# Performance work log

Measured on AMD Instinct MI355X. Metric: run time of the kernel, lower is better.

The kernel has to match this reference:

```python
import jax, jax.numpy as jnp
import numpy as np

N = 100000
E = 1600000
IN_DIM = 128
OUT_DIM = 64


def setup_inputs() -> dict:
    key = jax.random.key(0)
    k_h, k_ei, k_ew, k_W, k_a = jax.random.split(key, 5)
    h = jax.random.normal(k_h, (N, IN_DIM), dtype=jnp.float32)
    edge_index = jax.random.randint(k_ei, (2, E), 0, N, dtype=jnp.int64)
    edge_weight = jax.random.uniform(k_ew, (E,), dtype=jnp.float32)
    # nn.Linear weights (Kaiming-uniform-ish scale)
    W = jax.random.uniform(k_W, (OUT_DIM, IN_DIM), dtype=jnp.float32,
                           minval=-1.0, maxval=1.0) / np.sqrt(IN_DIM)
    a = jax.random.uniform(k_a, (2 * OUT_DIM,), dtype=jnp.float32,
                           minval=-1.0, maxval=1.0) / np.sqrt(2 * OUT_DIM)
    return {"h": h, "edge_index": edge_index, "edge_weight": edge_weight,
            "W": W, "a": a}


def reference(h, edge_index, edge_weight, W, a):
    # Faithful translation of _GATConvSparse.forward (inference; dropout = identity).
    n = h.shape[0]
    src, dst = edge_index[0], edge_index[1]
    Wh = h @ W.T                                  # (N, out_dim)
    d = Wh.shape[1]
    # a(cat([Wh[src], Wh[dst]])) == Wh[src] @ a[:d] + Wh[dst] @ a[d:]
    alpha = Wh[src] @ a[:d] + Wh[dst] @ a[d:]     # (E,)
    alpha = alpha * edge_weight
    # Buggy-but-faithful 'softmax': segment-sum raw scores onto dst nodes...
    alpha_node = jax.ops.segment_sum(alpha, dst, num_segments=n)   # (N,)
    alpha_exp = jnp.exp(alpha_node - alpha_node.max())             # (N,)
    # ...then normalize per-edge exp(src) by sum of exp(src) over each dst segment.
    denom = jax.ops.segment_sum(alpha_exp[src], dst, num_segments=n)  # (N,)
    alpha_norm = alpha_exp[src] / (denom[dst] + 1e-9)              # (E,)
    out = jax.ops.segment_sum(alpha_norm[:, None] * Wh[src], dst,
                              num_segments=n)                      # (N, out_dim)
    return jax.nn.elu(out)
```

## Files before the change

kernel.cpp:

```cpp
#include <hip/hip_runtime.h>
#include <math.h>

#define Nn 100000
#define Ee 1600000
#define IND 128
#define OUTD 64
#define DPB 64
#define NB 1563
#define BSTR 1536
#define CAP 1536
#define GB 1563
#define EB_BLOCKS 391
#define AFIX 1048576.0f

using bf16x8 = __attribute__((ext_vector_type(8))) short;
using f32x4 = __attribute__((ext_vector_type(4))) float;

__device__ __forceinline__ unsigned short f2bf(float f) {
    unsigned u = __float_as_uint(f);
    u = u + 0x7FFFu + ((u >> 16) & 1u);
    return (unsigned short)(u >> 16);
}
__device__ __forceinline__ float bf2f(unsigned short h) {
    return __uint_as_float(((unsigned)h) << 16);
}

__device__ __forceinline__ bool probe64(const void* __restrict__ ei) {
    const long long* p = (const long long*)ei;
    bool ok = true;
#pragma unroll
    for (int i = 0; i < 8; ++i) {
        long long v = p[i];
        ok = ok && (v >= 0 && v < Nn);
    }
    return ok;
}

__device__ __forceinline__ void load_edge(const void* ei, int e, bool is64,
                                          int& s, int& d) {
    if (is64) {
        const long long* p = (const long long*)ei;
        s = (int)p[e];
        d = (int)p[Ee + e];
    } else {
        const int* p = (const int*)ei;
        s = p[e];
        d = p[Ee + e];
    }
}

__global__ __launch_bounds__(256) void k_fused(
    const float* __restrict__ h, const float* __restrict__ W,
    const float* __restrict__ a, unsigned short* __restrict__ Whb,
    float* __restrict__ s1, float* __restrict__ s2) {
    __shared__ unsigned short Ash[64][136];
    __shared__ unsigned short Wsh[64][136];
    __shared__ float al[2 * OUTD];
    int bid = blockIdx.x;
    int t = threadIdx.x;

    int R = bid * 64;
    for (int i = t; i < 2048; i += 256) {
        float4 v = ((const float4*)W)[i];
        int r = i >> 5, c = (i & 31) << 2;
        unsigned lo = (unsigned)f2bf(v.x) | ((unsigned)f2bf(v.y) << 16);
        unsigned hi = (unsigned)f2bf(v.z) | ((unsigned)f2bf(v.w) << 16);
        *(uint2*)&Wsh[r][c] = make_uint2(lo, hi);
    }
    if (t < 32) ((float4*)al)[t] = ((const float4*)a)[t];
    for (int i = t; i < 2048; i += 256) {
        int r = i >> 5, c = (i & 31) << 2;
        int n = R + r;
        float4 v = make_float4(0.f, 0.f, 0.f, 0.f);
        if (n < Nn) v = ((const float4*)(h + (size_t)n * IND))[i & 31];
        unsigned lo = (unsigned)f2bf(v.x) | ((unsigned)f2bf(v.y) << 16);
        unsigned hi = (unsigned)f2bf(v.z) | ((unsigned)f2bf(v.w) << 16);
        *(uint2*)&Ash[r][c] = make_uint2(lo, hi);
    }
    __syncthreads();

    int w = t >> 6, l = t & 63;
    int li = l & 15, lg = l >> 4;
    f32x4 acc[4];
#pragma unroll
    for (int nt = 0; nt < 4; ++nt) acc[nt] = (f32x4){0.f, 0.f, 0.f, 0.f};
#pragma unroll
    for (int kk = 0; kk < 4; ++kk) {
        bf16x8 af = *(const bf16x8*)&Ash[w * 16 + li][kk * 32 + lg * 8];
#pragma unroll
        for (int nt = 0; nt < 4; ++nt) {
            bf16x8 bf = *(const bf16x8*)&Wsh[nt * 16 + li][kk * 32 + lg * 8];
            acc[nt] = __builtin_amdgcn_mfma_f32_16x16x32_bf16(af, bf,
                                                              acc[nt],
                                                              0, 0, 0);
        }
    }
    float p1[4] = {0.f, 0.f, 0.f, 0.f};
    float p2[4] = {0.f, 0.f, 0.f, 0.f};
#pragma unroll
    for (int nt = 0; nt < 4; ++nt) {
        float a1v = al[nt * 16 + li];
        float a2v = al[OUTD + nt * 16 + li];
#pragma unroll
        for (int r = 0; r < 4; ++r) {
            float v = acc[nt][r];
            p1[r] += v * a1v;
            p2[r] += v * a2v;
            int row = R + w * 16 + lg * 4 + r;
            if (row < Nn)
                Whb[(size_t)row * OUTD + nt * 16 + li] = f2bf(v);
        }
    }
#pragma unroll
    for (int r = 0; r < 4; ++r) {
#pragma unroll
        for (int m = 1; m < 16; m <<= 1) {
            p1[r] += __shfl_xor(p1[r], m, 64);
            p2[r] += __shfl_xor(p2[r], m, 64);
        }
    }
    if (li < 4) {
        int row = R + w * 16 + lg * 4 + li;
        if (row < Nn) {
            s1[row] = p1[li];
            s2[row] = p2[li];
        }
    }
}

__global__ __launch_bounds__(512) void k_binscatter(
    const void* __restrict__ ei, const float* __restrict__ ew,
    const float* __restrict__ s1, const float* __restrict__ s2,
    int* __restrict__ bcursor, uint2* __restrict__ bins) {
    __shared__ int cnt[NB];
    __shared__ int gbase[NB];
    for (int i = threadIdx.x; i < NB; i += 512) cnt[i] = 0;
    __syncthreads();
    bool is64 = probe64(ei);
    int base = blockIdx.x * 4096;
    unsigned rx[8];
    int ryi[8];
    int rb[8];
    int rk[8];
#pragma unroll
    for (int i = 0; i < 8; ++i) {
        int e = base + i * 512 + threadIdx.x;
        rb[i] = -1;
        rx[i] = 0;
        ryi[i] = 0;
        rk[i] = 0;
        if (e < Ee) {
            int s, d;
            load_edge(ei, e, is64, s, d);
            float alpha = (s1[s] + s2[d]) * ew[e];
            ryi[i] = (int)rintf(alpha * AFIX);
            int b = d >> 6;
            rb[i] = b;
            rk[i] = atomicAdd(&cnt[b], 1);
            rx[i] = ((unsigned)s << 7) | ((unsigned)(d & 63) << 24);
        }
    }
    __syncthreads();
    for (int i = threadIdx.x; i < NB; i += 512) {
        int c = cnt[i];
        if (c) gbase[i] = atomicAdd(bcursor + i, c);
    }
    __syncthreads();
#pragma unroll
    for (int i = 0; i < 8; ++i) {
        if (rb[i] >= 0) {
            int pos = gbase[rb[i]] + rk[i];
            if (pos < BSTR)
                bins[(size_t)rb[i] * BSTR + pos] =
                    make_uint2(rx[i], (unsigned)ryi[i]);
        }
    }
}

__global__ __launch_bounds__(256) void k_balpha(
    const uint2* __restrict__ bins, const int* __restrict__ bcnt,
    float* __restrict__ ae) {
    __shared__ int anl[DPB];
    int b = blockIdx.x;
    int t = threadIdx.x;
    if (t < DPB) anl[t] = 0;
    __syncthreads();
    int e0 = b * BSTR;
    int c = bcnt[b];
    int e1 = e0 + (c < BSTR ? c : BSTR);
    for (int k = e0 + t; k < e1; k += 256) {
        uint2 r = bins[k];
        atomicAdd(&anl[r.x >> 24], (int)r.y);
    }
    __syncthreads();
    if (t < DPB) {
        int n = b * DPB + t;
        if (n < Nn) ae[n] = expf((float)anl[t] * (1.f / AFIX));
    }
}

#define AGG_BODY(NR)                                                         \
    {                                                                        \
        uint2 rr[NR];                                                        \
        unsigned ww[NR];                                                     \
        _Pragma("unroll") for (int j = 0; j < NR; ++j)                       \
            rr[j] = lp[2 * j];                                               \
        _Pragma("unroll") for (int j = 0; j < NR; ++j)                       \
            ww[j] = *(const unsigned*)(whbB + (rr[j].x + hl4));              \
        _Pragma("unroll") for (int j = 0; j < NR; ++j) {                     \
            float aa = __uint_as_float(rr[j].y);                             \
            acc.x += aa * __uint_as_float(ww[j] << 16);                      \
            acc.y += aa * __uint_as_float(ww[j] & 0xFFFF0000u);              \
            den += aa;                                                       \
        }                                                                    \
        lp += 2 * NR;                                                        \
    }

__global__ __launch_bounds__(512, 4) void k_agg(
    const uint2* __restrict__ bins, const int* __restrict__ bcnt,
    const float* __restrict__ ae, const unsigned short* __restrict__ Whb,
    float* __restrict__ out) {
    __shared__ uint2 lrec[CAP];
    __shared__ int cnt[DPB];
    __shared__ int sbase[DPB];
    int b = blockIdx.x;
    int t = threadIdx.x;
    int lane = t & 63;
    int wave = t >> 6;
    int half = lane >> 5;
    int hl = lane & 31;
    unsigned hl4 = (unsigned)hl << 2;
    int e0 = b * BSTR;
    int c = bcnt[b];
    int total = c < BSTR ? c : BSTR;
    int e1 = e0 + total;
    const char* whbB = (const char*)Whb;

    if (t < DPB) cnt[t] = 0;
    __syncthreads();

    unsigned su[CAP / 512];
    float sa[CAP / 512];
    int srk[CAP / 512];
#pragma unroll
    for (int i = 0; i < CAP / 512; ++i) {
        int k = e0 + i * 512 + t;
        srk[i] = -1;
        if (k < e1) {
            uint2 r = bins[k];
            srk[i] = atomicAdd(&cnt[r.x >> 24], 1);
            su[i] = r.x;
            sa[i] = ae[(r.x >> 7) & 0x1FFFF];
        }
    }
    __syncthreads();
    if (t < DPB) {
        int v = cnt[t];
#pragma unroll
        for (int d = 1; d < DPB; d <<= 1) {
            int u = __shfl_up(v, d, 64);
            if (t >= d) v += u;
        }
        sbase[t] = v;
    }
    __syncthreads();
#pragma unroll
    for (int i = 0; i < CAP / 512; ++i) {
        if (srk[i] >= 0) {
            int dloc = su[i] >> 24;
            int pos = sbase[dloc] - cnt[dloc] + srk[i];
            lrec[pos] = make_uint2(su[i] & 0x00FFFF80u,
                                   __float_as_uint(sa[i]));
        }
    }
    __syncthreads();

    for (int d = wave * 8; d < wave * 8 + 8; ++d) {
        int k1 = sbase[d];
        int k = k1 - cnt[d];
        const uint2* lp = lrec + k + half;
        float2 acc = make_float2(0.f, 0.f);
        float den = 0.f;
        for (; k + 15 < k1; k += 16) AGG_BODY(8);
        for (; k + 7 < k1; k += 8) AGG_BODY(4);
        for (; k + 1 < k1; k += 2) AGG_BODY(1);
        if (k < k1) {
            uint2 rA = lrec[k];
            unsigned wA = *(const unsigned*)(whbB + (rA.x + hl4));
            float aA = half ? 0.f : __uint_as_float(rA.y);
            acc.x += aA * __uint_as_float(wA << 16);
            acc.y += aA * __uint_as_float(wA & 0xFFFF0000u);
            den += aA;
        }
        float ax = acc.x + __shfl_xor(acc.x, 32, 64);
        float ay = acc.y + __shfl_xor(acc.y, 32, 64);
        float dn = den + __shfl_xor(den, 32, 64);
        if (half == 0) {
            int n = b * DPB + d;
            if (n < Nn) {
                float inv = 1.f / (dn + 1e-9f);
                float vx = ax * inv;
                float vy = ay * inv;
                vx = vx > 0.f ? vx : expm1f(vx);
                vy = vy > 0.f ? vy : expm1f(vy);
                *(float2*)&out[(size_t)n * OUTD + hl * 2] =
                    make_float2(vx, vy);
            }
        }
    }
}

extern "C" void kernel_launch(void* const* d_in, const int* in_sizes, int n_in,
                              void* d_out, int out_size, void* d_ws,
                              size_t ws_size, hipStream_t stream) {
    const float* h = (const float*)d_in[0];
    const void* ei = d_in[1];
    const float* ew = (const float*)d_in[2];
    const float* W = (const float*)d_in[3];
    const float* a = (const float*)d_in[4];
    float* out = (float*)d_out;

    unsigned short* Whb = (unsigned short*)d_ws;
    float* s1 = (float*)(Whb + (size_t)Nn * OUTD);
    float* s2 = s1 + Nn;
    float* ae = s2 + Nn;
    int* bcursor = (int*)(ae + Nn);
    uint2* bins = (uint2*)(bcursor + 2048);

    hipMemsetAsync(bcursor, 0, 2048 * sizeof(int), stream);

    k_fused<<<GB, 256, 0, stream>>>(h, W, a, Whb, s1, s2);
    k_binscatter<<<EB_BLOCKS, 512, 0, stream>>>(ei, ew, s1, s2, bcursor, bins);
    k_balpha<<<NB, 256, 0, stream>>>(bins, bcursor, ae);
    k_agg<<<NB, 512, 0, stream>>>(bins, bcursor, ae, Whb, out);
}
```

Baseline: 107.6 us.

## Replace atomic bin cursors with a deterministic count-then-scan binning pass

Adds a histogram pass, fused into the matmul kernel as extra blocks, that counts edges per destination bin for each chunk. A new column-wise scan kernel turns those counts into per-chunk offsets, so the scatter kernel reads precomputed bases instead of doing global atomicAdds on shared cursors. This also removes the memset and shrinks the per-bin stride, giving a smaller bins buffer. The cost is an extra kernel launch, a second read of the destination indices, and a counts buffer in workspace.

```diff
diff --git a/kernel.cpp b/kernel.cpp
--- a/kernel.cpp
+++ b/kernel.cpp
@@ -7,10 +7,11 @@
 #define OUTD 64
 #define DPB 64
 #define NB 1563
-#define BSTR 1536
+#define BSTR 1280
 #define CAP 1536
 #define GB 1563
 #define EB_BLOCKS 391
+#define CSCAN_BLOCKS 196
 #define AFIX 1048576.0f
 
 using bf16x8 = __attribute__((ext_vector_type(8))) short;
@@ -49,95 +50,144 @@
     }
 }
 
+__device__ __forceinline__ int load_dst(const void* ei, int e, bool is64) {
+    if (is64) return (int)((const long long*)ei)[Ee + e];
+    return ((const int*)ei)[Ee + e];
+}
+
 __global__ __launch_bounds__(256) void k_fused(
     const float* __restrict__ h, const float* __restrict__ W,
     const float* __restrict__ a, unsigned short* __restrict__ Whb,
-    float* __restrict__ s1, float* __restrict__ s2) {
+    float* __restrict__ s1, float* __restrict__ s2,
+    const void* __restrict__ ei, unsigned short* __restrict__ counts) {
     __shared__ unsigned short Ash[64][136];
     __shared__ unsigned short Wsh[64][136];
     __shared__ float al[2 * OUTD];
     int bid = blockIdx.x;
     int t = threadIdx.x;
 
-    int R = bid * 64;
-    for (int i = t; i < 2048; i += 256) {
-        float4 v = ((const float4*)W)[i];
-        int r = i >> 5, c = (i & 31) << 2;
-        unsigned lo = (unsigned)f2bf(v.x) | ((unsigned)f2bf(v.y) << 16);
-        unsigned hi = (unsigned)f2bf(v.z) | ((unsigned)f2bf(v.w) << 16);
-        *(uint2*)&Wsh[r][c] = make_uint2(lo, hi);
-    }
-    if (t < 32) ((float4*)al)[t] = ((const float4*)a)[t];
-    for (int i = t; i < 2048; i += 256) {
-        int r = i >> 5, c = (i & 31) << 2;
-        int n = R + r;
-        float4 v = make_float4(0.f, 0.f, 0.f, 0.f);
-        if (n < Nn) v = ((const float4*)(h + (size_t)n * IND))[i & 31];
-        unsigned lo = (unsigned)f2bf(v.x) | ((unsigned)f2bf(v.y) << 16);
-        unsigned hi = (unsigned)f2bf(v.z) | ((unsigned)f2bf(v.w) << 16);
-        *(uint2*)&Ash[r][c] = make_uint2(lo, hi);
-    }
-    __syncthreads();
-
-    int w = t >> 6, l = t & 63;
-    int li = l & 15, lg = l >> 4;
-    f32x4 acc[4];
-#pragma unroll
-    for (int nt = 0; nt < 4; ++nt) acc[nt] = (f32x4){0.f, 0.f, 0.f, 0.f};
-#pragma unroll
-    for (int kk = 0; kk < 4; ++kk) {
-        bf16x8 af = *(const bf16x8*)&Ash[w * 16 + li][kk * 32 + lg * 8];
+    if (bid < GB) {
+        int R = bid * 64;
+        for (int i = t; i < 2048; i += 256) {
+            float4 v = ((const float4*)W)[i];
+            int r = i >> 5, c = (i & 31) << 2;
+            unsigned lo = (unsigned)f2bf(v.x) | ((unsigned)f2bf(v.y) << 16);
+            unsigned hi = (unsigned)f2bf(v.z) | ((unsigned)f2bf(v.w) << 16);
+            *(uint2*)&Wsh[r][c] = make_uint2(lo, hi);
+        }
+        if (t < 32) ((float4*)al)[t] = ((const float4*)a)[t];
+        for (int i = t; i < 2048; i += 256) {
+            int r = i >> 5, c = (i & 31) << 2;
+            int n = R + r;
+            float4 v = make_float4(0.f, 0.f, 0.f, 0.f);
+            if (n < Nn) v = ((const float4*)(h + (size_t)n * IND))[i & 31];
+            unsigned lo = (unsigned)f2bf(v.x) | ((unsigned)f2bf(v.y) << 16);
+            unsigned hi = (unsigned)f2bf(v.z) | ((unsigned)f2bf(v.w) << 16);
+            *(uint2*)&Ash[r][c] = make_uint2(lo, hi);
+        }
+        __syncthreads();
+
+        int w = t >> 6, l = t & 63;
+        int li = l & 15, lg = l >> 4;
+        f32x4 acc[4];
+#pragma unroll
+        for (int nt = 0; nt < 4; ++nt) acc[nt] = (f32x4){0.f, 0.f, 0.f, 0.f};
+#pragma unroll
+        for (int kk = 0; kk < 4; ++kk) {
+            bf16x8 af = *(const bf16x8*)&Ash[w * 16 + li][kk * 32 + lg * 8];
+#pragma unroll
+            for (int nt = 0; nt < 4; ++nt) {
+                bf16x8 bf = *(const bf16x8*)&Wsh[nt * 16 + li][kk * 32 + lg * 8];
+                acc[nt] = __builtin_amdgcn_mfma_f32_16x16x32_bf16(af, bf,
+                                                                  acc[nt],
+                                                                  0, 0, 0);
+            }
+        }
+        float p1[4] = {0.f, 0.f, 0.f, 0.f};
+        float p2[4] = {0.f, 0.f, 0.f, 0.f};
 #pragma unroll
         for (int nt = 0; nt < 4; ++nt) {
-            bf16x8 bf = *(const bf16x8*)&Wsh[nt * 16 + li][kk * 32 + lg * 8];
-            acc[nt] = __builtin_amdgcn_mfma_f32_16x16x32_bf16(af, bf,
-                                                              acc[nt],
-                                                              0, 0, 0);
-        }
-    }
-    float p1[4] = {0.f, 0.f, 0.f, 0.f};
-    float p2[4] = {0.f, 0.f, 0.f, 0.f};
-#pragma unroll
-    for (int nt = 0; nt < 4; ++nt) {
-        float a1v = al[nt * 16 + li];
-        float a2v = al[OUTD + nt * 16 + li];
+            float a1v = al[nt * 16 + li];
+            float a2v = al[OUTD + nt * 16 + li];
+#pragma unroll
+            for (int r = 0; r < 4; ++r) {
+                float v = acc[nt][r];
+                p1[r] += v * a1v;
+                p2[r] += v * a2v;
+                int row = R + w * 16 + lg * 4 + r;
+                if (row < Nn)
+                    Whb[(size_t)row * OUTD + nt * 16 + li] = f2bf(v);
+            }
+        }
 #pragma unroll
         for (int r = 0; r < 4; ++r) {
-            float v = acc[nt][r];
-            p1[r] += v * a1v;
-            p2[r] += v * a2v;
-            int row = R + w * 16 + lg * 4 + r;
-            if (row < Nn)
-                Whb[(size_t)row * OUTD + nt * 16 + li] = f2bf(v);
-        }
-    }
-#pragma unroll
-    for (int r = 0; r < 4; ++r) {
-#pragma unroll
-        for (int m = 1; m < 16; m <<= 1) {
-            p1[r] += __shfl_xor(p1[r], m, 64);
-            p2[r] += __shfl_xor(p2[r], m, 64);
-        }
-    }
-    if (li < 4) {
-        int row = R + w * 16 + lg * 4 + li;
-        if (row < Nn) {
-            s1[row] = p1[li];
-            s2[row] = p2[li];
-        }
-    }
+#pragma unroll
+            for (int m = 1; m < 16; m <<= 1) {
+                p1[r] += __shfl_xor(p1[r], m, 64);
+                p2[r] += __shfl_xor(p2[r], m, 64);
+            }
+        }
+        if (li < 4) {
+            int row = R + w * 16 + lg * 4 + li;
+            if (row < Nn) {
+                s1[row] = p1[li];
+                s2[row] = p2[li];
+            }
+        }
+    } else {
+        int* cnt = (int*)&Ash[0][0];
+        for (int i = t; i < NB; i += 256) cnt[i] = 0;
+        __syncthreads();
+        bool is64 = probe64(ei);
+        int hc = bid - GB;
+        int base = hc * 4096;
+#pragma unroll
+        for (int i = 0; i < 16; ++i) {
+            int e = base + i * 256 + t;
+            if (e < Ee) atomicAdd(&cnt[load_dst(ei, e, is64) >> 6], 1);
+        }
+        __syncthreads();
+        for (int i = t; i < NB; i += 256)
+            counts[(size_t)hc * NB + i] = (unsigned short)cnt[i];
+    }
+}
+
+__global__ __launch_bounds__(512) void k_cscan(
+    unsigned short* __restrict__ counts, int* __restrict__ bcnt) {
+    int gw = (int)((blockIdx.x * 512 + threadIdx.x) >> 6);
+    int lane = threadIdx.x & 63;
+    if (gw >= NB) return;
+    int run = 0;
+    for (int c0 = 0; c0 < EB_BLOCKS; c0 += 64) {
+        int c = c0 + lane;
+        int v = (c < EB_BLOCKS) ? (int)counts[(size_t)c * NB + gw] : 0;
+        int s = v;
+#pragma unroll
+        for (int d = 1; d < 64; d <<= 1) {
+            int u = __shfl_up(s, d, 64);
+            if (lane >= d) s += u;
+        }
+        if (c < EB_BLOCKS)
+            counts[(size_t)c * NB + gw] = (unsigned short)(run + s - v);
+        run += __shfl(s, 63, 64);
+    }
+    if (lane == 0) bcnt[gw] = run;
 }
 
 __global__ __launch_bounds__(512) void k_binscatter(
     const void* __restrict__ ei, const float* __restrict__ ew,
     const float* __restrict__ s1, const float* __restrict__ s2,
-    int* __restrict__ bcursor, uint2* __restrict__ bins) {
+    const unsigned short* __restrict__ counts, uint2* __restrict__ bins) {
     __shared__ int cnt[NB];
     __shared__ int gbase[NB];
-    for (int i = threadIdx.x; i < NB; i += 512) cnt[i] = 0;
+    int hc = blockIdx.x;
+    for (int i = threadIdx.x; i < NB; i += 512) {
+        cnt[i] = 0;
+        gbase[i] = (int)counts[(size_t)hc * NB + i];
+    }
     __syncthreads();
     bool is64 = probe64(ei);
-    int base = blockIdx.x * 4096;
+    int base = hc * 4096;
     unsigned rx[8];
     int ryi[8];
     int rb[8];
@@ -161,17 +211,12 @@
         }
     }
     __syncthreads();
-    for (int i = threadIdx.x; i < NB; i += 512) {
-        int c = cnt[i];
-        if (c) gbase[i] = atomicAdd(bcursor + i, c);
-    }
-    __syncthreads();
 #pragma unroll
     for (int i = 0; i < 8; ++i) {
         if (rb[i] >= 0) {
-            int pos = gbase[rb[i]] + rk[i];
-            if (pos < BSTR)
-                bins[(size_t)rb[i] * BSTR + pos] =
+            int off = gbase[rb[i]] + rk[i];
+            if (off < BSTR)
+                bins[(size_t)rb[i] * BSTR + off] =
                     make_uint2(rx[i], (unsigned)ryi[i]);
         }
     }
@@ -324,13 +369,15 @@
     float* s1 = (float*)(Whb + (size_t)Nn * OUTD);
     float* s2 = s1 + Nn;
     float* ae = s2 + Nn;
-    int* bcursor = (int*)(ae + Nn);
-    uint2* bins = (uint2*)(bcursor + 2048);
-
-    hipMemsetAsync(bcursor, 0, 2048 * sizeof(int), stream);
-
-    k_fused<<<GB, 256, 0, stream>>>(h, W, a, Whb, s1, s2);
-    k_binscatter<<<EB_BLOCKS, 512, 0, stream>>>(ei, ew, s1, s2, bcursor, bins);
-    k_balpha<<<NB, 256, 0, stream>>>(bins, bcursor, ae);
-    k_agg<<<NB, 512, 0, stream>>>(bins, bcursor, ae, Whb, out);
-}
+    int* bcnt = (int*)(ae + Nn);
+    uint2* bins = (uint2*)(bcnt + 2048);
+    unsigned short* counts =
+        (unsigned short*)(bins + (size_t)NB * BSTR);
+
+    k_fused<<<GB + EB_BLOCKS, 256, 0, stream>>>(h, W, a, Whb, s1, s2, ei,
+                                                counts);
+    k_cscan<<<CSCAN_BLOCKS, 512, 0, stream>>>(counts, bcnt);
+    k_binscatter<<<EB_BLOCKS, 512, 0, stream>>>(ei, ew, s1, s2, counts, bins);
+    k_balpha<<<NB, 256, 0, stream>>>(bins, bcnt, ae);
+    k_agg<<<NB, 512, 0, stream>>>(bins, bcnt, ae, Whb, out);
+}
```

New measurement: 110.2 us. 1.02x slower.
